# Performance work log

Measured on AMD Instinct MI355X. Metric: run time of the kernel, lower is better.

## Reference

```python
import jax, jax.numpy as jnp
import numpy as np

EMBED_DIM = 1024
NUM_HEADS = 16
HEAD_DIM = EMBED_DIM // NUM_HEADS  # 64
B, T = 4, 2048
ROPE_BASE = 10000.0


def rope_tables(T, head_dim):
    # matches RotaryPositionalEmbedding: inv_freq over even indices
    inv_freq = 1.0 / (ROPE_BASE ** (jnp.arange(0, head_dim, 2, dtype=jnp.float32) / head_dim))
    freqs = jnp.arange(T, dtype=jnp.float32)[:, None] * inv_freq[None, :]  # [T, head_dim//2]
    emb = jnp.concatenate([freqs, freqs], axis=-1)  # [T, head_dim]
    return jnp.cos(emb), jnp.sin(emb)


def apply_rotary(x, cos, sin):
    # x: [B, H, T, D]; cos/sin: [T, D] but only first D//2 cols used (as in torch code)
    d = x.shape[-1] // 2
    x1, x2 = x[..., :d], x[..., d:]
    c = cos[None, None, :, :d]
    s = sin[None, None, :, :d]
    return jnp.concatenate([x1 * c - x2 * s, x1 * s + x2 * c], axis=-1)


def setup_inputs() -> dict:
    key = jax.random.key(0)
    k1, k2, k3, k4 = jax.random.split(key, 4)
    x = jax.random.normal(k1, (B, T, EMBED_DIM), dtype=jnp.float32)
    attention_mask = jnp.ones((B, T), dtype=jnp.int32)
    W_qkv = jax.random.normal(k2, (EMBED_DIM, 3 * EMBED_DIM), dtype=jnp.float32) / np.sqrt(EMBED_DIM)
    W_out = jax.random.normal(k3, (EMBED_DIM, EMBED_DIM), dtype=jnp.float32) / np.sqrt(EMBED_DIM)
    b_out = jax.random.normal(k4, (EMBED_DIM,), dtype=jnp.float32) * 0.01
    return {"x": x, "attention_mask": attention_mask, "W_qkv": W_qkv, "W_out": W_out, "b_out": b_out}


def reference(x, attention_mask, W_qkv, W_out, b_out):
    Bq, Tq, C = x.shape
    H, D = NUM_HEADS, HEAD_DIM
    qkv = (x @ W_qkv).reshape(Bq, Tq, 3, H, D)
    qkv = jnp.transpose(qkv, (2, 0, 3, 1, 4))  # [3, B, H, T, D]
    q, k, v = qkv[0], qkv[1], qkv[2]

    cos, sin = rope_tables(Tq, D)
    q = apply_rotary(q, cos, sin)
    k = apply_rotary(k, cos, sin)

    scale = 1.0 / np.sqrt(D)
    attn = jnp.einsum('bhtd,bhsd->bhts', q, k) * scale  # [B, H, T, T]
    causal = jnp.tril(jnp.ones((Tq, Tq), dtype=bool))
    attn = jnp.where(causal[None, None], attn, -jnp.inf)
    pad = attention_mask[:, None, None, :] != 0  # [B,1,1,T]
    attn = jnp.where(pad, attn, -jnp.inf)
    attn = jax.nn.softmax(attn, axis=-1)
    out = jnp.einsum('bhts,bhsd->bthd', attn, v).reshape(Bq, Tq, C)
    return out @ W_out + b_out
```

## Files before the change

### kernel.cpp

```cpp
#include <hip/hip_runtime.h>
#include <hip/hip_bf16.h>
#include <math.h>

typedef __attribute__((ext_vector_type(8))) __bf16 bf16x8;
typedef __attribute__((ext_vector_type(4))) __bf16 bf16x4;
typedef __attribute__((ext_vector_type(4))) float f32x4;

#define B_ 4
#define T_ 2048
#define C_ 1024
#define H_ 16
#define D_ 64
#define M_TOT (B_*T_)

static __device__ __forceinline__ f32x4 mfma_bf16(bf16x8 a, bf16x8 b, f32x4 c) {
  return __builtin_amdgcn_mfma_f32_16x16x32_bf16(a, b, c, 0, 0, 0);
}

static __device__ __forceinline__ void gload_lds16(const void* g, void* l) {
  __builtin_amdgcn_global_load_lds((const __attribute__((address_space(1))) void*)g,
                                   (__attribute__((address_space(3))) void*)l, 16, 0, 0);
}

__global__ void prep_all(const float* __restrict__ x, __bf16* __restrict__ xb,
                         float* __restrict__ cosT, float* __restrict__ sinT,
                         const float* __restrict__ Wqkv, __bf16* __restrict__ wqkvT,
                         const float* __restrict__ Wout, __bf16* __restrict__ woutT) {
  __shared__ float tile[32][33];
  const int bid = blockIdx.x;
  if (bid < 8192) {
    int i = bid * 256 + threadIdx.x;
    float4 v = ((const float4*)x)[i];
    bf16x4 o = { (__bf16)v.x, (__bf16)v.y, (__bf16)v.z, (__bf16)v.w };
    *(bf16x4*)(xb + (size_t)i*4) = o;
  } else if (bid < 8448) {
    int idx = (bid - 8192) * 256 + threadIdx.x;
    int t = idx >> 5, d = idx & 31;
    float inv = powf(10000.0f, -((float)(2*d)) / 64.0f);
    float ang = (float)t * inv;
    cosT[idx] = cosf(ang);
    sinT[idx] = sinf(ang);
  } else {
    int tId = bid - 8448;
    const float* in;  __bf16* out;  int N, n0, k0;
    if (tId < 3072) { in = Wqkv; out = wqkvT; N = 3072; n0 = (tId % 96)*32; k0 = (tId / 96)*32; }
    else { tId -= 3072; in = Wout; out = woutT; N = 1024; n0 = (tId % 32)*32; k0 = (tId / 32)*32; }
    int tx = threadIdx.x & 31, ty = threadIdx.x >> 5;
    #pragma unroll
    for (int r = ty; r < 32; r += 8) tile[r][tx] = in[(size_t)(k0 + r)*N + n0 + tx];
    __syncthreads();
    #pragma unroll
    for (int r = ty; r < 32; r += 8) out[(size_t)(n0 + r)*1024 + k0 + tx] = (__bf16)tile[tx][r];
  }
}


#define GEMM_PHASES(N_TILES)                                                     \
  auto RD_BFR = [&](const char* lb, bf16x8 (*bfr)[2]) {                          \
    _Pragma("unroll")                                                            \
    for (int n = 0; n < 4; ++n) {                                                \
      const int row = wc*64 + n*16 + l15;                                        \
      const int sw = (row & 7) << 4;                                             \
      _Pragma("unroll")                                                          \
      for (int ks = 0; ks < 2; ++ks)                                             \
        bfr[n][ks] = *(const bf16x8*)(lb + row*128 + ((ks*64 + lhi*16) ^ sw));   \
    }                                                                            \
  };                                                                             \
  auto RD_AF = [&](const char* la, int mb, bf16x8 (*af)[2]) {                    \
    _Pragma("unroll")                                                            \
    for (int mm = 0; mm < 2; ++mm) {                                             \
      const int row = wr*64 + (mb + mm)*16 + l15;                                \
      const int sw = (row & 7) << 4;                                             \
      _Pragma("unroll")                                                          \
      for (int ks = 0; ks < 2; ++ks)                                             \
        af[mm][ks] = *(const bf16x8*)(la + row*128 + ((ks*64 + lhi*16) ^ sw));   \
    }                                                                            \
  };                                                                             \
  auto MFMA16 = [&](bf16x8 (*af)[2], bf16x8 (*bfr)[2], int mb) {                 \
    __builtin_amdgcn_s_setprio(1);                                               \
    _Pragma("unroll")                                                            \
    for (int mm = 0; mm < 2; ++mm)                                               \
      _Pragma("unroll")                                                          \
      for (int n = 0; n < 4; ++n)                                                \
        _Pragma("unroll")                                                        \
        for (int ks = 0; ks < 2; ++ks)                                           \
          acc[mb + mm][n] = mfma_bf16(af[mm][ks], bfr[n][ks], acc[mb + mm][n]);  \
    __builtin_amdgcn_s_setprio(0);                                               \
  };                                                                             \
  STAGE_B(0, (char*)lB[0]); STAGE_A(0, (char*)lA[0]); STAGE_B(1, (char*)lB[1]);  \
  asm volatile("s_waitcnt vmcnt(4)" ::: "memory");                               \
  __builtin_amdgcn_s_barrier();                                                  \
  _Pragma("unroll")                                                              \
  for (int it = 0; it < (N_TILES)/2; ++it) {                                     \
    const int t0 = it*2;                                                         \
    bf16x8 bfr[4][2], af[2][2];                                                  \
    RD_BFR((const char*)lB[0], bfr);                                             \
    RD_AF((const char*)lA[0], 0, af);                                            \
    STAGE_A(t0 + 1, (char*)lA[1]);                                               \
    __builtin_amdgcn_s_barrier();                                                \
    MFMA16(af, bfr, 0);                                                          \
    __builtin_amdgcn_s_barrier();                                                \
    RD_AF((const char*)lA[0], 2, af);                                            \
    if (t0 + 2 < (N_TILES)) STAGE_B(t0 + 2, (char*)lB[0]);                       \
    __builtin_amdgcn_s_barrier();                                                \
    MFMA16(af, bfr, 2);                                                          \
    if (t0 + 2 < (N_TILES)) asm volatile("s_waitcnt vmcnt(4)" ::: "memory");     \
    else                    asm volatile("s_waitcnt vmcnt(0)" ::: "memory");     \
    __builtin_amdgcn_s_barrier();                                                \
    RD_BFR((const char*)lB[1], bfr);                                             \
    RD_AF((const char*)lA[1], 0, af);                                            \
    if (t0 + 2 < (N_TILES)) STAGE_A(t0 + 2, (char*)lA[0]);                       \
    __builtin_amdgcn_s_barrier();                                                \
    MFMA16(af, bfr, 0);                                                          \
    __builtin_amdgcn_s_barrier();                                                \
    RD_AF((const char*)lA[1], 2, af);                                            \
    if (t0 + 3 < (N_TILES)) STAGE_B(t0 + 3, (char*)lB[1]);                       \
    __builtin_amdgcn_s_barrier();                                                \
    MFMA16(af, bfr, 2);                                                          \
    if (it < (N_TILES)/2 - 1) asm volatile("s_waitcnt vmcnt(4)" ::: "memory");   \
    __builtin_amdgcn_s_barrier();                                                \
  }

__global__ void __launch_bounds__(512, 2)
gemm_qkv_p(const __bf16* __restrict__ A, const __bf16* __restrict__ Bt,
           __bf16* __restrict__ qout, __bf16* __restrict__ kout, __bf16* __restrict__ vtout,
           const float* __restrict__ cosT, const float* __restrict__ sinT)
{
  __shared__ __attribute__((aligned(16))) char smem[98304];
  auto lA = (__bf16 (*)[128*64])smem;
  auto lB = (__bf16 (*)[256*64])(smem + 32768);
  const int tid = threadIdx.x;
  const int lane = tid & 63, wave = tid >> 6;
  const int wr = wave >> 2, wc = wave & 3;
  const int l15 = lane & 15, lhi = lane >> 4;

  const int id = blockIdx.x;
  const int xcd = id & 7, j = id >> 3;
  const int rowt = xcd*8 + (j & 7);
  const int row0 = rowt * 128;
  const int col0 = (j >> 3) * 256;

  f32x4 acc[4][4] = {};

  const char* Abase = (const char*)A + (size_t)row0 * 2048;
  const char* Bbase = (const char*)Bt + (size_t)col0 * 2048;

  auto STAGE_A = [&](int kt, char* dst) {
    #pragma unroll
    for (int c = 0; c < 2; ++c) {
      const int L = tid*16 + c*8192;
      const int row = L >> 7, colb = L & 127;
      const int sb = colb ^ ((row & 7) << 4);
      gload_lds16(Abase + (size_t)row*2048 + kt*128 + sb, dst + L);
    }
  };
  auto STAGE_B = [&](int kt, char* dst) {
    #pragma unroll
    for (int c = 0; c < 4; ++c) {
      const int L = tid*16 + c*8192;
      const int row = L >> 7, colb = L & 127;
      const int sb = colb ^ ((row & 7) << 4);
      gload_lds16(Bbase + (size_t)row*2048 + kt*128 + sb, dst + L);
    }
  };

  GEMM_PHASES(16)

  const int slot = (col0 >> 6) + wc;
  const int which = slot >> 4;
  const int h = slot & 15;
  if (which == 2) {
    __bf16* lTw = (__bf16*)(smem + wave*8320);
    #pragma unroll
    for (int m = 0; m < 4; ++m)
      #pragma unroll
      for (int r = 0; r < 4; ++r) {
        const int trow = m*16 + lhi*4 + r;
        #pragma unroll
        for (int n = 0; n < 4; ++n)
          lTw[trow*65 + n*16 + l15] = (__bf16)acc[m][n][r];
      }
    const int t0w = row0 + wr*64;
    const int b = t0w >> 11, tloc = t0w & 2047;
    __bf16* dstv = vtout + ((size_t)(b*H_ + h)*D_)*T_;
    #pragma unroll
    for (int c2 = 0; c2 < 8; ++c2) {
      const int idx = lane + c2*64;
      const int d = idx >> 3, t8 = (idx & 7)*8;
      bf16x8 ov;
      #pragma unroll
      for (int jj = 0; jj < 8; ++jj) ov[jj] = lTw[(t8 + jj)*65 + d];
      *(bf16x8*)(dstv + (size_t)d*T_ + tloc + t8) = ov;
    }
  } else {
    __bf16* dst = (which == 0) ? qout : kout;
    const float fsc = (which == 0) ? 0.18033688011112042f : 1.0f;
    #pragma unroll
    for (int m = 0; m < 4; ++m) {
      #pragma unroll
      for (int r = 0; r < 4; ++r) {
        const int grow = row0 + wr*64 + m*16 + lhi*4 + r;
        const int b = grow >> 11, t = grow & 2047;
        const size_t obase = ((size_t)(b*H_ + h)*T_ + t)*D_;
        #pragma unroll
        for (int n = 0; n < 2; ++n) {
          const int d1 = n*16 + l15;
          const float c = cosT[t*32 + d1];
          const float s = sinT[t*32 + d1];
          const float x1 = acc[m][n][r];
          const float x2 = acc[m][n+2][r];
          dst[obase + d1]      = (__bf16)((x1*c - x2*s) * fsc);
          dst[obase + d1 + 32] = (__bf16)((x1*s + x2*c) * fsc);
        }
      }
    }
  }
}

__global__ void __launch_bounds__(512, 2)
gemm_out_p(const __bf16* __restrict__ A, const __bf16* __restrict__ Bt,
           float* __restrict__ fout, const float* __restrict__ bias)
{
  __shared__ __attribute__((aligned(16))) __bf16 lA[2][128*64];
  __shared__ __attribute__((aligned(16))) __bf16 lB[2][256*64];
  const int tid = threadIdx.x;
  const int lane = tid & 63, wave = tid >> 6;
  const int wr = wave >> 2, wc = wave & 3;
  const int l15 = lane & 15, lhi = lane >> 4;

  const int id = blockIdx.x;
  const int xcd = id & 7, j = id >> 3;
  const int rowt = xcd*8 + (j & 7);
  const int row0 = rowt * 128;
  const int col0 = (j >> 3) * 256;

  f32x4 acc[4][4] = {};

  const char* Abase = (const char*)A + (size_t)row0 * 2048;
  const char* Bbase = (const char*)Bt + (size_t)col0 * 2048;

  auto STAGE_A = [&](int kt, char* dst) {
    #pragma unroll
    for (int c = 0; c < 2; ++c) {
      const int L = tid*16 + c*8192;
      const int row = L >> 7, colb = L & 127;
      const int sb = colb ^ ((row & 7) << 4);
      gload_lds16(Abase + (size_t)row*2048 + kt*128 + sb, dst + L);
    }
  };
  auto STAGE_B = [&](int kt, char* dst) {
    #pragma unroll
    for (int c = 0; c < 4; ++c) {
      const int L = tid*16 + c*8192;
      const int row = L >> 7, colb = L & 127;
      const int sb = colb ^ ((row & 7) << 4);
      gload_lds16(Bbase + (size_t)row*2048 + kt*128 + sb, dst + L);
    }
  };

  GEMM_PHASES(16)

  #pragma unroll
  for (int m = 0; m < 4; ++m) {
    #pragma unroll
    for (int r = 0; r < 4; ++r) {
      const int grow = row0 + wr*64 + m*16 + lhi*4 + r;
      #pragma unroll
      for (int n = 0; n < 4; ++n) {
        const int gcol = col0 + wc*64 + n*16 + l15;
        fout[(size_t)grow*1024 + gcol] = acc[m][n][r] + bias[gcol];
      }
    }
  }
}

#define THR_LOG2 8.0f

static __device__ const char QB_TAB[24] = {15,15,7,14,14,13,13,6,12,12,11,11,5,10,10,9,9,4,8,8,3,2,1,0};
static __device__ const char SP_TAB[24] = { 0, 1,2, 0, 1, 0, 1,2, 0, 1, 0, 1,2, 0, 1,0,1,2,0,1,2,2,2,2};

__global__ void __launch_bounds__(256, 3)
attn_kernel(const __bf16* __restrict__ q, const __bf16* __restrict__ k,
            const __bf16* __restrict__ vt, const int* __restrict__ amask,
            __bf16* __restrict__ aout,
            __bf16* __restrict__ pO, float* __restrict__ pM, float* __restrict__ pL)
{
  __shared__ __attribute__((aligned(16))) __bf16 lK[64*64];
  __shared__ __attribute__((aligned(16))) __bf16 lVt[64*64];
  __shared__ __attribute__((aligned(16))) __bf16 lP[4][32*64];
  const int tid = threadIdx.x;
  const int lane = tid & 63, wave = tid >> 6;
  const int l15 = lane & 15, lhi = lane >> 4;

  const int g = blockIdx.x >> 6;
  const int bh = blockIdx.x & 63;
  const int qblock = QB_TAB[g];
  const int sp = SP_TAB[g];
  const int kb0   = (sp == 1) ? (qblock + 1) : 0;
  const int kbend = (sp == 0) ? (qblock + 1) : (2*qblock + 2);

  const int b = bh >> 4, h = bh & 15;
  const size_t kvbase = (size_t)bh * T_ * D_;
  const char* kbase  = (const char*)(k + kvbase);
  const char* vtbase = (const char*)(vt + kvbase);
  char* lPw = (char*)lP[wave];

  const int q0w = qblock*128 + wave*32;

  bf16x8 aq[2][2];
  #pragma unroll
  for (int m = 0; m < 2; ++m)
    #pragma unroll
    for (int ks = 0; ks < 2; ++ks)
      aq[m][ks] = *(const bf16x8*)(q + kvbase + (size_t)(q0w + m*16 + l15)*D_ + ks*32 + lhi*8);

  f32x4 acc_o[2][4] = {};
  f32x4 acc_l[2] = {};
  float m_w = -3e37f;

  for (int kb = kb0; kb < kbend; ++kb) {
    #pragma unroll
    for (int c = 0; c < 2; ++c) {
      const int L = tid*16 + c*4096;
      const int row = L >> 7;
      const int sb  = (L & 127) ^ ((row & 7) << 4);
      gload_lds16(kbase  + (size_t)(kb*64 + row)*128 + sb, (char*)lK + L);
      gload_lds16(vtbase + (size_t)row*(T_*2) + (size_t)kb*128 + sb, (char*)lVt + L);
    }
    __syncthreads();

    if (kb*64 <= q0w + 31) {
      const char* lKc = (const char*)lK;
      const char* lVc = (const char*)lVt;

      const unsigned long long pm = __ballot(amask[b*T_ + kb*64 + lane] != 0);

      f32x4 sc[2][4] = {};
      __builtin_amdgcn_s_setprio(1);
      #pragma unroll
      for (int n = 0; n < 4; ++n) {
        const int row = n*16 + l15;
        const int sw = (row & 7) << 4;
        #pragma unroll
        for (int ks = 0; ks < 2; ++ks) {
          bf16x8 bk = *(const bf16x8*)(lKc + row*128 + ((ks*64 + lhi*16) ^ sw));
          #pragma unroll
          for (int m = 0; m < 2; ++m)
            sc[m][n] = mfma_bf16(bk, aq[m][ks], sc[m][n]);
        }
      }
      __builtin_amdgcn_s_setprio(0);

      if (kb*64 + 63 > q0w) {
        #pragma unroll
        for (int m = 0; m < 2; ++m) {
          const int qv = q0w + m*16 + l15;
          #pragma unroll
          for (int n = 0; n < 4; ++n)
            #pragma unroll
            for (int r = 0; r < 4; ++r)
              if (kb*64 + n*16 + lhi*4 + r > qv) sc[m][n][r] = -3e37f;
        }
      }

      f32x4 vm = sc[0][0];
      #pragma unroll
      for (int m = 0; m < 2; ++m)
        #pragma unroll
        for (int n = 0; n < 4; ++n) {
          if (m == 0 && n == 0) continue;
          #pragma unroll
          for (int r = 0; r < 4; ++r) vm[r] = fmaxf(vm[r], sc[m][n][r]);
        }
      float tmax = fmaxf(fmaxf(vm[0], vm[1]), fmaxf(vm[2], vm[3]));
      #pragma unroll
      for (int off = 1; off < 64; off <<= 1)
        tmax = fmaxf(tmax, __shfl_xor(tmax, off));

      if (tmax > m_w + THR_LOG2) {
        const float corr = __builtin_amdgcn_exp2f(m_w - tmax);
        #pragma unroll
        for (int m = 0; m < 2; ++m) {
          #pragma unroll
          for (int c = 0; c < 4; ++c) acc_o[m][c] *= corr;
          acc_l[m] *= corr;
        }
        m_w = tmax;
      }

      float mkv[4][4];
      #pragma unroll
      for (int n = 0; n < 4; ++n)
        #pragma unroll
        for (int r = 0; r < 4; ++r) mkv[n][r] = m_w;
      if (pm != ~0ull) {
        #pragma unroll
        for (int n = 0; n < 4; ++n)
          #pragma unroll
          for (int r = 0; r < 4; ++r)
            if (!((pm >> (n*16 + lhi*4 + r)) & 1)) mkv[n][r] = 3e37f;
      }

      const int swq = (l15 & 7) << 4;
      #pragma unroll
      for (int m = 0; m < 2; ++m) {
        char* prow = lPw + (m*16 + l15)*128;
        #pragma unroll
        for (int n = 0; n < 4; ++n) {
          bf16x4 pk;
          #pragma unroll
          for (int r = 0; r < 4; ++r)
            pk[r] = (__bf16)__builtin_amdgcn_exp2f(sc[m][n][r] - mkv[n][r]);
          *(bf16x4*)(prow + ((32*n + 8*lhi) ^ swq)) = pk;
        }
      }

      bf16x8 pa[2][2];
      #pragma unroll
      for (int m = 0; m < 2; ++m) {
        const int row = m*16 + l15;
        const int sw = (row & 7) << 4;
        #pragma unroll
        for (int ks = 0; ks < 2; ++ks)
          pa[m][ks] = *(const bf16x8*)(lPw + row*128 + ((ks*64 + lhi*16) ^ sw));
      }

      __builtin_amdgcn_s_setprio(1);
      const __bf16 one = (__bf16)1.0f;
      const bf16x8 vone = {one, one, one, one, one, one, one, one};
      #pragma unroll
      for (int m = 0; m < 2; ++m)
        #pragma unroll
        for (int ks = 0; ks < 2; ++ks)
          acc_l[m] = mfma_bf16(pa[m][ks], vone, acc_l[m]);

      #pragma unroll
      for (int c = 0; c < 4; ++c) {
        const int row = c*16 + l15;
        const int sw = (row & 7) << 4;
        #pragma unroll
        for (int ks = 0; ks < 2; ++ks) {
          bf16x8 bv = *(const bf16x8*)(lVc + row*128 + ((ks*64 + lhi*16) ^ sw));
          #pragma unroll
          for (int m = 0; m < 2; ++m)
            acc_o[m][c] = mfma_bf16(pa[m][ks], bv, acc_o[m][c]);
        }
      }
      __builtin_amdgcn_s_setprio(0);
    }
    __syncthreads();
  }

  if (sp == 2) {
    #pragma unroll
    for (int m = 0; m < 2; ++m)
      #pragma unroll
      for (int r = 0; r < 4; ++r) {
        const int tq = q0w + m*16 + lhi*4 + r;
        const float invl = 1.0f / acc_l[m][r];
        const size_t obase = ((size_t)b*T_ + tq)*C_ + h*D_;
        #pragma unroll
        for (int c = 0; c < 4; ++c)
          aout[obase + c*16 + l15] = (__bf16)(acc_o[m][c][r] * invl);
      }
  } else {
    const int pidx = ((qblock - 8)*2 + sp)*64 + bh;
    __bf16* po = pO + (size_t)pidx*128*64;
    float* pm2 = pM + pidx*128;
    float* pl = pL + pidx*128;
    #pragma unroll
    for (int m = 0; m < 2; ++m)
      #pragma unroll
      for (int r = 0; r < 4; ++r) {
        const int rw = wave*32 + m*16 + lhi*4 + r;
        if (l15 == 0) { pm2[rw] = m_w; pl[rw] = acc_l[m][r]; }
        #pragma unroll
        for (int c = 0; c < 4; ++c)
          po[(size_t)rw*64 + c*16 + l15] = (__bf16)acc_o[m][c][r];
      }
  }
}

__global__ void __launch_bounds__(256)
attn_combine(const __bf16* __restrict__ pO, const float* __restrict__ pM,
             const float* __restrict__ pL, __bf16* __restrict__ aout)
{
  const int g = blockIdx.x;
  const int qb8 = g >> 6, bh = g & 63;
  const int p0 = (qb8*2)*64 + bh, p1 = (qb8*2 + 1)*64 + bh;
  const int row = threadIdx.x >> 1, ch = threadIdx.x & 1;
  const float m0 = pM[p0*128 + row], m1 = pM[p1*128 + row];
  const float l0 = pL[p0*128 + row], l1 = pL[p1*128 + row];
  const float M = fmaxf(m0, m1);
  const float w0 = __builtin_amdgcn_exp2f(m0 - M);
  const float w1 = __builtin_amdgcn_exp2f(m1 - M);
  const float inv = 1.0f / (l0*w0 + l1*w1);
  const int b = bh >> 4, h = bh & 15;
  const int t = (qb8 + 8)*128 + row;
  const __bf16* o0 = pO + ((size_t)p0*128 + row)*64 + ch*32;
  const __bf16* o1 = pO + ((size_t)p1*128 + row)*64 + ch*32;
  __bf16* dst = aout + ((size_t)b*T_ + t)*C_ + h*D_ + ch*32;
  #pragma unroll
  for (int j = 0; j < 32; j += 8) {
    bf16x8 a = *(const bf16x8*)(o0 + j);
    bf16x8 c = *(const bf16x8*)(o1 + j);
    bf16x8 rr;
    #pragma unroll
    for (int e = 0; e < 8; ++e)
      rr[e] = (__bf16)(((float)a[e]*w0 + (float)c[e]*w1) * inv);
    *(bf16x8*)(dst + j) = rr;
  }
}


extern "C" void kernel_launch(void* const* d_in, const int* in_sizes, int n_in,
                              void* d_out, int out_size, void* d_ws, size_t ws_size,
                              hipStream_t stream)
{
  const float* x     = (const float*)d_in[0];
  const int*   amask = (const int*)d_in[1];
  const float* Wqkv  = (const float*)d_in[2];
  const float* Wout  = (const float*)d_in[3];
  const float* bout  = (const float*)d_in[4];
  float* out = (float*)d_out;

  char* w = (char*)d_ws;
  __bf16* xb    = (__bf16*)w;  w += (size_t)M_TOT*C_*2;
  __bf16* wqkvT = (__bf16*)w;  w += (size_t)3072*1024*2;
  __bf16* woutT = (__bf16*)w;  w += (size_t)1024*1024*2;
  __bf16* qb    = (__bf16*)w;  w += (size_t)B_*H_*T_*D_*2;
  __bf16* kb    = (__bf16*)w;  w += (size_t)B_*H_*T_*D_*2;
  __bf16* vtb   = (__bf16*)w;  w += (size_t)B_*H_*T_*D_*2;
  __bf16* aob   = (__bf16*)w;  w += (size_t)M_TOT*C_*2;
  float*  cosT  = (float*)w;   w += (size_t)T_*32*4;
  float*  sinT  = (float*)w;   w += (size_t)T_*32*4;
  __bf16* pO    = (__bf16*)w;  w += (size_t)1024*128*64*2;
  float*  pM    = (float*)w;   w += (size_t)1024*128*4;
  float*  pL    = (float*)w;   w += (size_t)1024*128*4;

  prep_all<<<dim3(8192 + 256 + 3072 + 1024), 256, 0, stream>>>(
      x, xb, cosT, sinT, Wqkv, wqkvT, Wout, woutT);

  gemm_qkv_p<<<dim3(768), 512, 0, stream>>>(xb, wqkvT, qb, kb, vtb, cosT, sinT);

  attn_kernel<<<dim3(1536), 256, 0, stream>>>(qb, kb, vtb, amask, aob, pO, pM, pL);
  attn_combine<<<dim3(512), 256, 0, stream>>>(pO, pM, pL, aob);

  gemm_out_p<<<dim3(256), 512, 0, stream>>>(aob, woutT, out, bout);
}
```

Baseline: 165.1 us.

## Drop split-KV attention and combine kernel; one block per query tile

Replaces the split-K attention schedule, which used lookup tables, partial outputs and a separate combine kernel, with a plain schedule of one block per 128-row query tile, ordered longest-first. Each block runs over all of its causal key blocks and writes the normalized output directly. This removes the partial-output traffic and one kernel launch. In exchange the largest query tiles are no longer split across blocks, so tail imbalance may grow. The padding-mask path is also reorganized into separate fast and masked branches.

```diff
diff --git a/kernel.cpp b/kernel.cpp
--- a/kernel.cpp
+++ b/kernel.cpp
@@ -276,14 +276,10 @@
 
 #define THR_LOG2 8.0f
 
-static __device__ const char QB_TAB[24] = {15,15,7,14,14,13,13,6,12,12,11,11,5,10,10,9,9,4,8,8,3,2,1,0};
-static __device__ const char SP_TAB[24] = { 0, 1,2, 0, 1, 0, 1,2, 0, 1, 0, 1,2, 0, 1,0,1,2,0,1,2,2,2,2};
-
 __global__ void __launch_bounds__(256, 3)
 attn_kernel(const __bf16* __restrict__ q, const __bf16* __restrict__ k,
             const __bf16* __restrict__ vt, const int* __restrict__ amask,
-            __bf16* __restrict__ aout,
-            __bf16* __restrict__ pO, float* __restrict__ pM, float* __restrict__ pL)
+            __bf16* __restrict__ aout)
 {
   __shared__ __attribute__((aligned(16))) __bf16 lK[64*64];
   __shared__ __attribute__((aligned(16))) __bf16 lVt[64*64];
@@ -292,12 +288,9 @@
   const int lane = tid & 63, wave = tid >> 6;
   const int l15 = lane & 15, lhi = lane >> 4;
 
-  const int g = blockIdx.x >> 6;
+  const int qblock = 15 - (blockIdx.x >> 6);
   const int bh = blockIdx.x & 63;
-  const int qblock = QB_TAB[g];
-  const int sp = SP_TAB[g];
-  const int kb0   = (sp == 1) ? (qblock + 1) : 0;
-  const int kbend = (sp == 0) ? (qblock + 1) : (2*qblock + 2);
+  const int kbend = 2*qblock + 2;
 
   const int b = bh >> 4, h = bh & 15;
   const size_t kvbase = (size_t)bh * T_ * D_;
@@ -318,7 +311,7 @@
   f32x4 acc_l[2] = {};
   float m_w = -3e37f;
 
-  for (int kb = kb0; kb < kbend; ++kb) {
+  for (int kb = 0; kb < kbend; ++kb) {
     #pragma unroll
     for (int c = 0; c < 2; ++c) {
       const int L = tid*16 + c*4096;
@@ -388,30 +381,34 @@
         m_w = tmax;
       }
 
-      float mkv[4][4];
-      #pragma unroll
-      for (int n = 0; n < 4; ++n)
-        #pragma unroll
-        for (int r = 0; r < 4; ++r) mkv[n][r] = m_w;
-      if (pm != ~0ull) {
-        #pragma unroll
-        for (int n = 0; n < 4; ++n)
-          #pragma unroll
-          for (int r = 0; r < 4; ++r)
-            if (!((pm >> (n*16 + lhi*4 + r)) & 1)) mkv[n][r] = 3e37f;
-      }
-
       const int swq = (l15 & 7) << 4;
-      #pragma unroll
-      for (int m = 0; m < 2; ++m) {
-        char* prow = lPw + (m*16 + l15)*128;
-        #pragma unroll
-        for (int n = 0; n < 4; ++n) {
-          bf16x4 pk;
-          #pragma unroll
-          for (int r = 0; r < 4; ++r)
-            pk[r] = (__bf16)__builtin_amdgcn_exp2f(sc[m][n][r] - mkv[n][r]);
-          *(bf16x4*)(prow + ((32*n + 8*lhi) ^ swq)) = pk;
+      if (pm == ~0ull) {
+        #pragma unroll
+        for (int m = 0; m < 2; ++m) {
+          char* prow = lPw + (m*16 + l15)*128;
+          #pragma unroll
+          for (int n = 0; n < 4; ++n) {
+            bf16x4 pk;
+            #pragma unroll
+            for (int r = 0; r < 4; ++r)
+              pk[r] = (__bf16)__builtin_amdgcn_exp2f(sc[m][n][r] - m_w);
+            *(bf16x4*)(prow + ((32*n + 8*lhi) ^ swq)) = pk;
+          }
+        }
+      } else {
+        #pragma unroll
+        for (int m = 0; m < 2; ++m) {
+          char* prow = lPw + (m*16 + l15)*128;
+          #pragma unroll
+          for (int n = 0; n < 4; ++n) {
+            bf16x4 pk;
+            #pragma unroll
+            for (int r = 0; r < 4; ++r) {
+              const float sub = ((pm >> (n*16 + lhi*4 + r)) & 1) ? m_w : 3e37f;
+              pk[r] = (__bf16)__builtin_amdgcn_exp2f(sc[m][n][r] - sub);
+            }
+            *(bf16x4*)(prow + ((32*n + 8*lhi) ^ swq)) = pk;
+          }
         }
       }
 
@@ -451,65 +448,17 @@
     __syncthreads();
   }
 
-  if (sp == 2) {
-    #pragma unroll
-    for (int m = 0; m < 2; ++m)
-      #pragma unroll
-      for (int r = 0; r < 4; ++r) {
-        const int tq = q0w + m*16 + lhi*4 + r;
-        const float invl = 1.0f / acc_l[m][r];
-        const size_t obase = ((size_t)b*T_ + tq)*C_ + h*D_;
-        #pragma unroll
-        for (int c = 0; c < 4; ++c)
-          aout[obase + c*16 + l15] = (__bf16)(acc_o[m][c][r] * invl);
-      }
-  } else {
-    const int pidx = ((qblock - 8)*2 + sp)*64 + bh;
-    __bf16* po = pO + (size_t)pidx*128*64;
-    float* pm2 = pM + pidx*128;
-    float* pl = pL + pidx*128;
-    #pragma unroll
-    for (int m = 0; m < 2; ++m)
-      #pragma unroll
-      for (int r = 0; r < 4; ++r) {
-        const int rw = wave*32 + m*16 + lhi*4 + r;
-        if (l15 == 0) { pm2[rw] = m_w; pl[rw] = acc_l[m][r]; }
-        #pragma unroll
-        for (int c = 0; c < 4; ++c)
-          po[(size_t)rw*64 + c*16 + l15] = (__bf16)acc_o[m][c][r];
-      }
-  }
-}
-
-__global__ void __launch_bounds__(256)
-attn_combine(const __bf16* __restrict__ pO, const float* __restrict__ pM,
-             const float* __restrict__ pL, __bf16* __restrict__ aout)
-{
-  const int g = blockIdx.x;
-  const int qb8 = g >> 6, bh = g & 63;
-  const int p0 = (qb8*2)*64 + bh, p1 = (qb8*2 + 1)*64 + bh;
-  const int row = threadIdx.x >> 1, ch = threadIdx.x & 1;
-  const float m0 = pM[p0*128 + row], m1 = pM[p1*128 + row];
-  const float l0 = pL[p0*128 + row], l1 = pL[p1*128 + row];
-  const float M = fmaxf(m0, m1);
-  const float w0 = __builtin_amdgcn_exp2f(m0 - M);
-  const float w1 = __builtin_amdgcn_exp2f(m1 - M);
-  const float inv = 1.0f / (l0*w0 + l1*w1);
-  const int b = bh >> 4, h = bh & 15;
-  const int t = (qb8 + 8)*128 + row;
-  const __bf16* o0 = pO + ((size_t)p0*128 + row)*64 + ch*32;
-  const __bf16* o1 = pO + ((size_t)p1*128 + row)*64 + ch*32;
-  __bf16* dst = aout + ((size_t)b*T_ + t)*C_ + h*D_ + ch*32;
   #pragma unroll
-  for (int j = 0; j < 32; j += 8) {
-    bf16x8 a = *(const bf16x8*)(o0 + j);
-    bf16x8 c = *(const bf16x8*)(o1 + j);
-    bf16x8 rr;
-    #pragma unroll
-    for (int e = 0; e < 8; ++e)
-      rr[e] = (__bf16)(((float)a[e]*w0 + (float)c[e]*w1) * inv);
-    *(bf16x8*)(dst + j) = rr;
-  }
+  for (int m = 0; m < 2; ++m)
+    #pragma unroll
+    for (int r = 0; r < 4; ++r) {
+      const int tq = q0w + m*16 + lhi*4 + r;
+      const float invl = 1.0f / acc_l[m][r];
+      const size_t obase = ((size_t)b*T_ + tq)*C_ + h*D_;
+      #pragma unroll
+      for (int c = 0; c < 4; ++c)
+        aout[obase + c*16 + l15] = (__bf16)(acc_o[m][c][r] * invl);
+    }
 }
 
 
@@ -534,17 +483,13 @@
   __bf16* aob   = (__bf16*)w;  w += (size_t)M_TOT*C_*2;
   float*  cosT  = (float*)w;   w += (size_t)T_*32*4;
   float*  sinT  = (float*)w;   w += (size_t)T_*32*4;
-  __bf16* pO    = (__bf16*)w;  w += (size_t)1024*128*64*2;
-  float*  pM    = (float*)w;   w += (size_t)1024*128*4;
-  float*  pL    = (float*)w;   w += (size_t)1024*128*4;
 
   prep_all<<<dim3(8192 + 256 + 3072 + 1024), 256, 0, stream>>>(
       x, xb, cosT, sinT, Wqkv, wqkvT, Wout, woutT);
 
   gemm_qkv_p<<<dim3(768), 512, 0, stream>>>(xb, wqkvT, qb, kb, vtb, cosT, sinT);
 
-  attn_kernel<<<dim3(1536), 256, 0, stream>>>(qb, kb, vtb, amask, aob, pO, pM, pL);
-  attn_combine<<<dim3(512), 256, 0, stream>>>(pO, pM, pL, aob);
+  attn_kernel<<<dim3(1024), 256, 0, stream>>>(qb, kb, vtb, amask, aob);
 
   gemm_out_p<<<dim3(256), 512, 0, stream>>>(aob, woutT, out, bout);
 }
```

After: 162.6 us (median of 2 runs). About the same (-1.5%).
